# Optimization experiments

Measured on AMD Instinct MI355X. Metric: run time of the kernel, lower is better.

The kernel has to match this reference:

```python
import jax, jax.numpy as jnp
import numpy as np

# Ground-plane grid from proj_2DTo2D: W = 640/4 = 160, H = 480/4 = 120
GP_H, GP_W = 120, 160
PATCH_NUM = 1


def setup_inputs() -> dict:
    key = jax.random.key(0)
    k1, k2, k3 = jax.random.split(key, 3)
    nR, fh, fw, fdim = 4, 90, 160, 512  # 4 camera views, quarter-res feature maps
    nV = GP_H * GP_W  # 19200 ground-plane points per view
    inputs = jax.random.normal(k1, (nR, fh, fw, fdim), dtype=jnp.float32)
    # Projected image-plane coordinates (stand-in for calibration-based World2Image)
    im_x = jax.random.uniform(k2, (nR, nV), dtype=jnp.float32) * (fw - 1)
    im_y = jax.random.uniform(k3, (nR, nV), dtype=jnp.float32) * (fh - 1)
    return {"inputs": inputs, "im_x": im_x, "im_y": im_y}


def reference(inputs, im_x, im_y):
    # inputs: [nR, fh, fw, fdim]; im_x/im_y: [nR, nV] float pixel coords
    nR, fh, fw, fdim = inputs.shape
    im_x = jnp.clip(im_x, 0.0, fw - 1)
    im_y = jnp.clip(im_y, 0.0, fh - 1)
    x0 = jnp.floor(im_x).astype(jnp.int32)
    x1 = jnp.clip(x0 + 1, 0, fw - 1)
    y0 = jnp.floor(im_y).astype(jnp.int32)
    y1 = jnp.clip(y0 + 1, 0, fh - 1)
    x0f, x1f = x0.astype(im_x.dtype), x1.astype(im_x.dtype)
    y0f, y1f = y0.astype(im_y.dtype), y1.astype(im_y.dtype)

    b = jnp.arange(nR)[:, None]  # [nR, 1] batch index per grid point
    Ia = inputs[b, y0, x0]  # [nR, nV, fdim]
    Ib = inputs[b, y1, x0]
    Ic = inputs[b, y0, x1]
    Id = inputs[b, y1, x1]

    wa = ((x1f - im_x) * (y1f - im_y))[..., None]
    wb = ((x1f - im_x) * (im_y - y0f))[..., None]
    wc = ((im_x - x0f) * (y1f - im_y))[..., None]
    wd = ((im_x - x0f) * (im_y - y0f))[..., None]

    Ibilin = wa * Ia + wb * Ib + wc * Ic + wd * Id  # [nR, nV, fdim]
    return Ibilin.reshape(nR // PATCH_NUM, PATCH_NUM, GP_H, GP_W, fdim)
```

## Files before the change

kernel.cpp:

```cpp
#include <hip/hip_runtime.h>


typedef float f32x4 __attribute__((ext_vector_type(4)));

#define GLOBAL_AS __attribute__((address_space(1)))
#define LDS_AS    __attribute__((address_space(3)))

constexpr int NR   = 4;
constexpr int FH   = 90;
constexpr int FW   = 160;
constexpr int FDIM = 512;
constexpr int NV   = 120 * 160;
constexpr int NPTS = NR * NV;
constexpr int C4   = FDIM / 4;

constexpr int BY   = 2;
constexpr int BX   = 5;
constexpr int NGY  = FH / BY;
constexpr int NGX  = FW / BX;
constexpr int NBINS = NR * NGY * NGX;
constexpr int SY   = BY + 1;
constexpr int SX   = BX + 1;
constexpr int SCELLS = SY * SX;
constexpr int LDSX4 = SCELLS * C4;

constexpr int CAP   = 32;
constexpr int OVCAP = 4096;
constexpr int TPB   = 512;

__global__ void k_scatter(const float* __restrict__ imx, const float* __restrict__ imy,
                          int* __restrict__ binCnt, int* __restrict__ ovCnt,
                          int* __restrict__ perm, float2* __restrict__ sXY,
                          int* __restrict__ ovList) {
    int pt = blockIdx.x * blockDim.x + threadIdx.x;
    if (pt >= NPTS) return;
    int r = pt / NV;
    float x = fminf(fmaxf(imx[pt], 0.0f), (float)(FW - 1));
    float y = fminf(fmaxf(imy[pt], 0.0f), (float)(FH - 1));
    int b = (r * NGY + (int)floorf(y) / BY) * NGX + (int)floorf(x) / BX;
    int slot = atomicAdd(&binCnt[b], 1);
    if (slot < CAP) {
        int idx = b * CAP + slot;
        perm[idx] = pt;
        sXY[idx] = make_float2(x, y);
    } else {
        int o = atomicAdd(ovCnt, 1);
        if (o < OVCAP) ovList[o] = pt;
    }
}

__device__ __forceinline__ f32x4 lerp4(f32x4 A, f32x4 B, f32x4 C, f32x4 D,
                                       float wa, float wb, float wc, float wd) {
    return wa * A + wb * B + wc * C + wd * D;
}

__device__ __forceinline__ void weights_and_cells(float x, float y,
                                                  int& x0, int& x1, int& y0, int& y1,
                                                  float& wa, float& wb, float& wc, float& wd) {
    float x0f = floorf(x), y0f = floorf(y);
    x0 = (int)x0f; y0 = (int)y0f;
    x1 = min(x0 + 1, FW - 1);
    y1 = min(y0 + 1, FH - 1);
    float wx1 = (float)x1 - x;
    float wx0 = x - x0f;
    float wy1 = (float)y1 - y;
    float wy0 = y - y0f;
    wa = wx1 * wy1; wb = wx1 * wy0; wc = wx0 * wy1; wd = wx0 * wy0;
}

__global__ __launch_bounds__(TPB) void st_bins(
    const float* __restrict__ inp,
    const int* __restrict__ binCnt,
    const int* __restrict__ ovCnt,
    const int* __restrict__ perm,
    const float2* __restrict__ sXY,
    const int* __restrict__ ovList,
    const float* __restrict__ imx,
    const float* __restrict__ imy,
    float* __restrict__ out)
{
    __shared__ f32x4  lds[LDSX4];
    __shared__ int    pmS[CAP];
    __shared__ float2 xyS[CAP];

    int p = blockIdx.x;
    int b = (p & 7) * (NBINS >> 3) + (p >> 3);

    int r   = b / (NGY * NGX);
    int by0 = (b / NGX % NGY) * BY;
    int bx0 = (b % NGX) * BX;
    int tid = threadIdx.x;

    const f32x4* in4 = (const f32x4*)inp;
    int cnt  = min(binCnt[b], CAP);
    int base = b * CAP;

    #pragma unroll
    for (int i = 0; i < 5; ++i) {
        int idx = tid + i * TPB;
        if (idx < LDSX4) {
            int cell = idx >> 7;
            int c4   = idx & (C4 - 1);
            int ry   = cell / SX;
            int rx   = cell - ry * SX;
            int gy   = min(by0 + ry, FH - 1);
            int gx   = min(bx0 + rx, FW - 1);
            __builtin_amdgcn_global_load_lds(
                (const GLOBAL_AS void*)(in4 + (size_t)((r * FH + gy) * FW + gx) * C4 + c4),
                (LDS_AS void*)&lds[idx], 16, 0, 0);
        }
    }
    if (tid < cnt) {
        pmS[tid] = perm[base + tid];
        xyS[tid] = sXY[base + tid];
    }
    __syncthreads();

    int g  = tid >> 7;
    int c4 = tid & (C4 - 1);
    f32x4* out4 = (f32x4*)out;

    int i = g;
    for (; i + 4 < cnt; i += 8) {
        int    ptA = pmS[i];
        float2 cA  = xyS[i];
        int    ptB = pmS[i + 4];
        float2 cB  = xyS[i + 4];

        int x0A, x1A, y0A, y1A, x0B, x1B, y0B, y1B;
        float waA, wbA, wcA, wdA, waB, wbB, wcB, wdB;
        weights_and_cells(cA.x, cA.y, x0A, x1A, y0A, y1A, waA, wbA, wcA, wdA);
        weights_and_cells(cB.x, cB.y, x0B, x1B, y0B, y1B, waB, wbB, wcB, wdB);

        f32x4 Aa = lds[(((y0A - by0) * SX + (x0A - bx0)) << 7) + c4];
        f32x4 Ab = lds[(((y1A - by0) * SX + (x0A - bx0)) << 7) + c4];
        f32x4 Ac = lds[(((y0A - by0) * SX + (x1A - bx0)) << 7) + c4];
        f32x4 Ad = lds[(((y1A - by0) * SX + (x1A - bx0)) << 7) + c4];
        f32x4 Ba = lds[(((y0B - by0) * SX + (x0B - bx0)) << 7) + c4];
        f32x4 Bb = lds[(((y1B - by0) * SX + (x0B - bx0)) << 7) + c4];
        f32x4 Bc = lds[(((y0B - by0) * SX + (x1B - bx0)) << 7) + c4];
        f32x4 Bd = lds[(((y1B - by0) * SX + (x1B - bx0)) << 7) + c4];

        __builtin_nontemporal_store(lerp4(Aa, Ab, Ac, Ad, waA, wbA, wcA, wdA),
                                    out4 + (size_t)ptA * C4 + c4);
        __builtin_nontemporal_store(lerp4(Ba, Bb, Bc, Bd, waB, wbB, wcB, wdB),
                                    out4 + (size_t)ptB * C4 + c4);
    }
    if (i < cnt) {
        int    pt = pmS[i];
        float2 cc = xyS[i];
        int x0, x1, y0, y1; float wa, wb, wc, wd;
        weights_and_cells(cc.x, cc.y, x0, x1, y0, y1, wa, wb, wc, wd);
        f32x4 A = lds[(((y0 - by0) * SX + (x0 - bx0)) << 7) + c4];
        f32x4 B = lds[(((y1 - by0) * SX + (x0 - bx0)) << 7) + c4];
        f32x4 C = lds[(((y0 - by0) * SX + (x1 - bx0)) << 7) + c4];
        f32x4 D = lds[(((y1 - by0) * SX + (x1 - bx0)) << 7) + c4];
        __builtin_nontemporal_store(lerp4(A, B, C, D, wa, wb, wc, wd),
                                    out4 + (size_t)pt * C4 + c4);
    }

    int ov = min(*ovCnt, OVCAP);
    for (int j = b; j < ov; j += NBINS) {
        if (g != 0) continue;
        int pt = ovList[j];
        int rr = pt / NV;
        float x = fminf(fmaxf(imx[pt], 0.0f), (float)(FW - 1));
        float y = fminf(fmaxf(imy[pt], 0.0f), (float)(FH - 1));
        int x0, x1, y0, y1; float wa, wb, wc, wd;
        weights_and_cells(x, y, x0, x1, y0, y1, wa, wb, wc, wd);
        int rb = rr * FH;
        f32x4 A = in4[(size_t)((rb + y0) * FW + x0) * C4 + c4];
        f32x4 B = in4[(size_t)((rb + y1) * FW + x0) * C4 + c4];
        f32x4 C = in4[(size_t)((rb + y0) * FW + x1) * C4 + c4];
        f32x4 D = in4[(size_t)((rb + y1) * FW + x1) * C4 + c4];
        __builtin_nontemporal_store(lerp4(A, B, C, D, wa, wb, wc, wd),
                                    out4 + (size_t)pt * C4 + c4);
    }
}

__global__ __launch_bounds__(256) void st_bilinear_direct(
    const float* __restrict__ inp,
    const float* __restrict__ imx,
    const float* __restrict__ imy,
    float* __restrict__ out)
{
    int gid = blockIdx.x * blockDim.x + threadIdx.x;
    int pt = gid >> 7;
    int c4 = gid & (C4 - 1);
    if (pt >= NPTS) return;
    int r = pt / NV;
    float x = fminf(fmaxf(imx[pt], 0.0f), (float)(FW - 1));
    float y = fminf(fmaxf(imy[pt], 0.0f), (float)(FH - 1));
    int x0, x1, y0, y1; float wa, wb, wc, wd;
    weights_and_cells(x, y, x0, x1, y0, y1, wa, wb, wc, wd);
    const f32x4* base = (const f32x4*)inp;
    int rb = r * FH;
    f32x4 a = base[(size_t)((rb + y0) * FW + x0) * C4 + c4];
    f32x4 b = base[(size_t)((rb + y1) * FW + x0) * C4 + c4];
    f32x4 c = base[(size_t)((rb + y0) * FW + x1) * C4 + c4];
    f32x4 d = base[(size_t)((rb + y1) * FW + x1) * C4 + c4];
    ((f32x4*)out)[(size_t)pt * C4 + c4] = lerp4(a, b, c, d, wa, wb, wc, wd);
}

extern "C" void kernel_launch(void* const* d_in, const int* in_sizes, int n_in,
                              void* d_out, int out_size, void* d_ws, size_t ws_size,
                              hipStream_t stream) {
    const float* inp = (const float*)d_in[0];
    const float* imx = (const float*)d_in[1];
    const float* imy = (const float*)d_in[2];
    float* out = (float*)d_out;

    size_t need = (size_t)(NBINS + 1 + NBINS * CAP + OVCAP) * sizeof(int)
                + (size_t)NBINS * CAP * sizeof(float2);

    if (ws_size < need) {
        int nblocks = (NPTS * C4) / 256;
        hipLaunchKernelGGL(st_bilinear_direct, dim3(nblocks), dim3(256), 0, stream,
                           inp, imx, imy, out);
        return;
    }

    int*    binCnt = (int*)d_ws;
    int*    ovCnt  = binCnt + NBINS;
    int*    perm   = ovCnt + 1;
    float2* sXY    = (float2*)(perm + (size_t)NBINS * CAP);
    int*    ovList = (int*)(sXY + (size_t)NBINS * CAP);

    hipMemsetAsync(binCnt, 0, (NBINS + 1) * sizeof(int), stream);
    hipLaunchKernelGGL(k_scatter, dim3((NPTS + 255) / 256), dim3(256), 0, stream,
                       imx, imy, binCnt, ovCnt, perm, sXY, ovList);
    hipLaunchKernelGGL(st_bins, dim3(NBINS), dim3(TPB), 0, stream,
                       inp, binCnt, ovCnt, perm, sXY, ovList, imx, imy, out);
}
```

Baseline: 58.60 us.

## Fuse memset, scatter and binned bilinear into one cooperative persistent kernel

```diff
diff --git a/kernel.cpp b/kernel.cpp
--- a/kernel.cpp
+++ b/kernel.cpp
@@ -1,5 +1,8 @@
 #include <hip/hip_runtime.h>
-
+#include <hip/hip_cooperative_groups.h>
+
+
+namespace cg = cooperative_groups;
 
 typedef float f32x4 __attribute__((ext_vector_type(4)));
 
@@ -19,6 +22,7 @@
 constexpr int NGY  = FH / BY;
 constexpr int NGX  = FW / BX;
 constexpr int NBINS = NR * NGY * NGX;
+constexpr int NBX  = NBINS / 8;
 constexpr int SY   = BY + 1;
 constexpr int SX   = BX + 1;
 constexpr int SCELLS = SY * SX;
@@ -27,6 +31,181 @@
 constexpr int CAP   = 32;
 constexpr int OVCAP = 4096;
 constexpr int TPB   = 512;
+
+__device__ __forceinline__ f32x4 lerp4(f32x4 A, f32x4 B, f32x4 C, f32x4 D,
+                                       float wa, float wb, float wc, float wd) {
+    return wa * A + wb * B + wc * C + wd * D;
+}
+
+__device__ __forceinline__ void weights_and_cells(float x, float y,
+                                                  int& x0, int& x1, int& y0, int& y1,
+                                                  float& wa, float& wb, float& wc, float& wd) {
+    float x0f = floorf(x), y0f = floorf(y);
+    x0 = (int)x0f; y0 = (int)y0f;
+    x1 = min(x0 + 1, FW - 1);
+    y1 = min(y0 + 1, FH - 1);
+    float wx1 = (float)x1 - x;
+    float wx0 = x - x0f;
+    float wy1 = (float)y1 - y;
+    float wy0 = y - y0f;
+    wa = wx1 * wy1; wb = wx1 * wy0; wc = wx0 * wy1; wd = wx0 * wy0;
+}
+
+__device__ __forceinline__ void stage_bin_dev(const f32x4* __restrict__ in4,
+                                              f32x4* ldsbuf, int b, int tid) {
+    int r   = b / (NGY * NGX);
+    int by0 = (b / NGX % NGY) * BY;
+    int bx0 = (b % NGX) * BX;
+    #pragma unroll
+    for (int i = 0; i < 5; ++i) {
+        int idx = tid + i * TPB;
+        if (idx < LDSX4) {
+            int cell = idx >> 7;
+            int cc   = idx & (C4 - 1);
+            int ry   = cell / SX;
+            int rx   = cell - ry * SX;
+            int gy   = min(by0 + ry, FH - 1);
+            int gx   = min(bx0 + rx, FW - 1);
+            __builtin_amdgcn_global_load_lds(
+                (const GLOBAL_AS void*)(in4 + (size_t)((r * FH + gy) * FW + gx) * C4 + cc),
+                (LDS_AS void*)&ldsbuf[idx], 16, 0, 0);
+        }
+    }
+}
+
+__global__ __launch_bounds__(TPB) void st_fused(
+    const float* __restrict__ inp,
+    const float* __restrict__ imx,
+    const float* __restrict__ imy,
+    int* __restrict__ binCnt,
+    int* __restrict__ ovCnt,
+    int* __restrict__ perm,
+    float2* __restrict__ sXY,
+    int* __restrict__ ovList,
+    float* __restrict__ out)
+{
+    __shared__ f32x4  lds[LDSX4];
+    __shared__ int    pmS[CAP];
+    __shared__ float2 xyS[CAP];
+
+    cg::grid_group grid = cg::this_grid();
+    int nblk = gridDim.x;
+    int nthreads = nblk * TPB;
+    int bid = blockIdx.x;
+    int tid = threadIdx.x;
+    int gt  = bid * TPB + tid;
+
+    const f32x4* in4 = (const f32x4*)inp;
+
+    int xcd = bid & 7;
+    int s   = bid >> 3;
+    int bpx = nblk >> 3;
+    int s0  = (s * NBX) / bpx;
+    int s1  = ((s + 1) * NBX) / bpx;
+
+    for (int i = gt; i < NBINS + 1; i += nthreads) binCnt[i] = 0;
+    __threadfence();
+    grid.sync();
+
+    stage_bin_dev(in4, lds, xcd * NBX + s0, tid);
+
+    for (int pt = gt; pt < NPTS; pt += nthreads) {
+        int r = pt / NV;
+        float x = fminf(fmaxf(imx[pt], 0.0f), (float)(FW - 1));
+        float y = fminf(fmaxf(imy[pt], 0.0f), (float)(FH - 1));
+        int b = (r * NGY + (int)floorf(y) / BY) * NGX + (int)floorf(x) / BX;
+        int slot = atomicAdd(&binCnt[b], 1);
+        if (slot < CAP) {
+            int idx = b * CAP + slot;
+            perm[idx] = pt;
+            sXY[idx] = make_float2(x, y);
+        } else {
+            int o = atomicAdd(ovCnt, 1);
+            if (o < OVCAP) ovList[o] = pt;
+        }
+    }
+    __threadfence();
+    grid.sync();
+
+    f32x4* out4 = (f32x4*)out;
+    int g  = tid >> 7;
+    int c4 = tid & (C4 - 1);
+
+    for (int k = s0; k < s1; ++k) {
+        int b = xcd * NBX + k;
+        if (k > s0)
+            stage_bin_dev(in4, lds, b, tid);
+
+        int by0 = (b / NGX % NGY) * BY;
+        int bx0 = (b % NGX) * BX;
+        int cnt  = min(binCnt[b], CAP);
+        int base = b * CAP;
+        if (tid < cnt) {
+            pmS[tid] = perm[base + tid];
+            xyS[tid] = sXY[base + tid];
+        }
+        __syncthreads();
+
+        int i = g;
+        for (; i + 4 < cnt; i += 8) {
+            int    ptA = pmS[i];
+            float2 cA  = xyS[i];
+            int    ptB = pmS[i + 4];
+            float2 cB  = xyS[i + 4];
+
+            int x0A, x1A, y0A, y1A, x0B, x1B, y0B, y1B;
+            float waA, wbA, wcA, wdA, waB, wbB, wcB, wdB;
+            weights_and_cells(cA.x, cA.y, x0A, x1A, y0A, y1A, waA, wbA, wcA, wdA);
+            weights_and_cells(cB.x, cB.y, x0B, x1B, y0B, y1B, waB, wbB, wcB, wdB);
+
+            f32x4 Aa = lds[(((y0A - by0) * SX + (x0A - bx0)) << 7) + c4];
+            f32x4 Ab = lds[(((y1A - by0) * SX + (x0A - bx0)) << 7) + c4];
+            f32x4 Ac = lds[(((y0A - by0) * SX + (x1A - bx0)) << 7) + c4];
+            f32x4 Ad = lds[(((y1A - by0) * SX + (x1A - bx0)) << 7) + c4];
+            f32x4 Ba = lds[(((y0B - by0) * SX + (x0B - bx0)) << 7) + c4];
+            f32x4 Bb = lds[(((y1B - by0) * SX + (x0B - bx0)) << 7) + c4];
+            f32x4 Bc = lds[(((y0B - by0) * SX + (x1B - bx0)) << 7) + c4];
+            f32x4 Bd = lds[(((y1B - by0) * SX + (x1B - bx0)) << 7) + c4];
+
+            __builtin_nontemporal_store(lerp4(Aa, Ab, Ac, Ad, waA, wbA, wcA, wdA),
+                                        out4 + (size_t)ptA * C4 + c4);
+            __builtin_nontemporal_store(lerp4(Ba, Bb, Bc, Bd, waB, wbB, wcB, wdB),
+                                        out4 + (size_t)ptB * C4 + c4);
+        }
+        if (i < cnt) {
+            int    pt = pmS[i];
+            float2 cc = xyS[i];
+            int x0, x1, y0, y1; float wa, wb, wc, wd;
+            weights_and_cells(cc.x, cc.y, x0, x1, y0, y1, wa, wb, wc, wd);
+            f32x4 A = lds[(((y0 - by0) * SX + (x0 - bx0)) << 7) + c4];
+            f32x4 B = lds[(((y1 - by0) * SX + (x0 - bx0)) << 7) + c4];
+            f32x4 C = lds[(((y0 - by0) * SX + (x1 - bx0)) << 7) + c4];
+            f32x4 D = lds[(((y1 - by0) * SX + (x1 - bx0)) << 7) + c4];
+            __builtin_nontemporal_store(lerp4(A, B, C, D, wa, wb, wc, wd),
+                                        out4 + (size_t)pt * C4 + c4);
+        }
+        __syncthreads();
+    }
+
+    int ov = min(*ovCnt, OVCAP);
+    for (int j = bid; j < ov; j += nblk) {
+        if (g != 0) continue;
+        int pt = ovList[j];
+        int rr = pt / NV;
+        float x = fminf(fmaxf(imx[pt], 0.0f), (float)(FW - 1));
+        float y = fminf(fmaxf(imy[pt], 0.0f), (float)(FH - 1));
+        int x0, x1, y0, y1; float wa, wb, wc, wd;
+        weights_and_cells(x, y, x0, x1, y0, y1, wa, wb, wc, wd);
+        int rb = rr * FH;
+        f32x4 A = in4[(size_t)((rb + y0) * FW + x0) * C4 + c4];
+        f32x4 B = in4[(size_t)((rb + y1) * FW + x0) * C4 + c4];
+        f32x4 C = in4[(size_t)((rb + y0) * FW + x1) * C4 + c4];
+        f32x4 D = in4[(size_t)((rb + y1) * FW + x1) * C4 + c4];
+        __builtin_nontemporal_store(lerp4(A, B, C, D, wa, wb, wc, wd),
+                                    out4 + (size_t)pt * C4 + c4);
+    }
+}
+
 
 __global__ void k_scatter(const float* __restrict__ imx, const float* __restrict__ imy,
                           int* __restrict__ binCnt, int* __restrict__ ovCnt,
@@ -49,25 +228,6 @@
     }
 }
 
-__device__ __forceinline__ f32x4 lerp4(f32x4 A, f32x4 B, f32x4 C, f32x4 D,
-                                       float wa, float wb, float wc, float wd) {
-    return wa * A + wb * B + wc * C + wd * D;
-}
-
-__device__ __forceinline__ void weights_and_cells(float x, float y,
-                                                  int& x0, int& x1, int& y0, int& y1,
-                                                  float& wa, float& wb, float& wc, float& wd) {
-    float x0f = floorf(x), y0f = floorf(y);
-    x0 = (int)x0f; y0 = (int)y0f;
-    x1 = min(x0 + 1, FW - 1);
-    y1 = min(y0 + 1, FH - 1);
-    float wx1 = (float)x1 - x;
-    float wx0 = x - x0f;
-    float wy1 = (float)y1 - y;
-    float wy0 = y - y0f;
-    wa = wx1 * wy1; wb = wx1 * wy0; wc = wx0 * wy1; wd = wx0 * wy0;
-}
-
 __global__ __launch_bounds__(TPB) void st_bins(
     const float* __restrict__ inp,
     const int* __restrict__ binCnt,
@@ -86,7 +246,6 @@
     int p = blockIdx.x;
     int b = (p & 7) * (NBINS >> 3) + (p >> 3);
 
-    int r   = b / (NGY * NGX);
     int by0 = (b / NGX % NGY) * BY;
     int bx0 = (b % NGX) * BX;
     int tid = threadIdx.x;
@@ -95,21 +254,7 @@
     int cnt  = min(binCnt[b], CAP);
     int base = b * CAP;
 
-    #pragma unroll
-    for (int i = 0; i < 5; ++i) {
-        int idx = tid + i * TPB;
-        if (idx < LDSX4) {
-            int cell = idx >> 7;
-            int c4   = idx & (C4 - 1);
-            int ry   = cell / SX;
-            int rx   = cell - ry * SX;
-            int gy   = min(by0 + ry, FH - 1);
-            int gx   = min(bx0 + rx, FW - 1);
-            __builtin_amdgcn_global_load_lds(
-                (const GLOBAL_AS void*)(in4 + (size_t)((r * FH + gy) * FW + gx) * C4 + c4),
-                (LDS_AS void*)&lds[idx], 16, 0, 0);
-        }
-    }
+    stage_bin_dev(in4, lds, b, tid);
     if (tid < cnt) {
         pmS[tid] = perm[base + tid];
         xyS[tid] = sXY[base + tid];
@@ -210,8 +355,8 @@
     const float* imy = (const float*)d_in[2];
     float* out = (float*)d_out;
 
-    size_t need = (size_t)(NBINS + 1 + NBINS * CAP + OVCAP) * sizeof(int)
-                + (size_t)NBINS * CAP * sizeof(float2);
+    size_t need = (size_t)NBINS * CAP * sizeof(float2)
+                + (size_t)(NBINS * CAP + NBINS + 1 + OVCAP) * sizeof(int);
 
     if (ws_size < need) {
         int nblocks = (NPTS * C4) / 256;
@@ -220,13 +365,33 @@
         return;
     }
 
-    int*    binCnt = (int*)d_ws;
+    float2* sXY    = (float2*)d_ws;
+    int*    perm   = (int*)(sXY + (size_t)NBINS * CAP);
+    int*    binCnt = perm + (size_t)NBINS * CAP;
     int*    ovCnt  = binCnt + NBINS;
-    int*    perm   = ovCnt + 1;
-    float2* sXY    = (float2*)(perm + (size_t)NBINS * CAP);
-    int*    ovList = (int*)(sXY + (size_t)NBINS * CAP);
-
-    hipMemsetAsync(binCnt, 0, (NBINS + 1) * sizeof(int), stream);
+    int*    ovList = ovCnt + 1;
+
+    int dev = 0, coop = 0, ncu = 0, bpc = 0;
+    (void)hipGetDevice(&dev);
+    (void)hipDeviceGetAttribute(&coop, hipDeviceAttributeCooperativeLaunch, dev);
+    (void)hipDeviceGetAttribute(&ncu, hipDeviceAttributeMultiprocessorCount, dev);
+    hipError_t oe = hipOccupancyMaxActiveBlocksPerMultiprocessor(
+        &bpc, (const void*)st_fused, TPB, 0);
+
+    if (coop && oe == hipSuccess && ncu > 0 && bpc > 0) {
+        int nblk = (ncu * bpc) & ~7;
+        if (nblk > 1024) nblk = 1024;
+        if (nblk >= 8) {
+            void* args[] = { (void*)&inp, (void*)&imx, (void*)&imy,
+                             (void*)&binCnt, (void*)&ovCnt, (void*)&perm,
+                             (void*)&sXY, (void*)&ovList, (void*)&out };
+            hipError_t le = hipLaunchCooperativeKernel(
+                (const void*)st_fused, dim3(nblk), dim3(TPB), args, 0, stream);
+            if (le == hipSuccess) return;
+        }
+    }
+
+    (void)hipMemsetAsync(binCnt, 0, (NBINS + 1) * sizeof(int), stream);
     hipLaunchKernelGGL(k_scatter, dim3((NPTS + 255) / 256), dim3(256), 0, stream,
                        imx, imy, binCnt, ovCnt, perm, sXY, ovList);
     hipLaunchKernelGGL(st_bins, dim3(NBINS), dim3(TPB), 0, stream,
```

Result: slower. 214.9 us (+266.7%).

## Split each bin across two half-channel blocks and move overflow to separate kernel

Applied to the files above, without the earlier changes.

```diff
diff --git a/kernel.cpp b/kernel.cpp
--- a/kernel.cpp
+++ b/kernel.cpp
@@ -13,20 +13,22 @@
 constexpr int NV   = 120 * 160;
 constexpr int NPTS = NR * NV;
 constexpr int C4   = FDIM / 4;
+constexpr int H4   = C4 / 2;
 
 constexpr int BY   = 2;
 constexpr int BX   = 5;
 constexpr int NGY  = FH / BY;
 constexpr int NGX  = FW / BX;
 constexpr int NBINS = NR * NGY * NGX;
+constexpr int NB2  = NBINS * 2;
 constexpr int SY   = BY + 1;
 constexpr int SX   = BX + 1;
 constexpr int SCELLS = SY * SX;
-constexpr int LDSX4 = SCELLS * C4;
+constexpr int LDSH = SCELLS * H4;
 
 constexpr int CAP   = 32;
 constexpr int OVCAP = 4096;
-constexpr int TPB   = 512;
+constexpr int TPB   = 256;
 
 __global__ void k_scatter(const float* __restrict__ imx, const float* __restrict__ imy,
                           int* __restrict__ binCnt, int* __restrict__ ovCnt,
@@ -68,23 +70,23 @@
     wa = wx1 * wy1; wb = wx1 * wy0; wc = wx0 * wy1; wd = wx0 * wy0;
 }
 
-__global__ __launch_bounds__(TPB) void st_bins(
+__global__ __launch_bounds__(TPB) void st_bins_half(
     const float* __restrict__ inp,
     const int* __restrict__ binCnt,
     const int* __restrict__ ovCnt,
     const int* __restrict__ perm,
     const float2* __restrict__ sXY,
     const int* __restrict__ ovList,
-    const float* __restrict__ imx,
-    const float* __restrict__ imy,
     float* __restrict__ out)
 {
-    __shared__ f32x4  lds[LDSX4];
+    __shared__ f32x4  lds[LDSH];
     __shared__ int    pmS[CAP];
     __shared__ float2 xyS[CAP];
 
     int p = blockIdx.x;
-    int b = (p & 7) * (NBINS >> 3) + (p >> 3);
+    int l    = (p & 7) * (NB2 >> 3) + (p >> 3);
+    int b    = l >> 1;
+    int half = l & 1;
 
     int r   = b / (NGY * NGX);
     int by0 = (b / NGX % NGY) * BY;
@@ -94,19 +96,20 @@
     const f32x4* in4 = (const f32x4*)inp;
     int cnt  = min(binCnt[b], CAP);
     int base = b * CAP;
+    int hofs = half * H4;
 
     #pragma unroll
     for (int i = 0; i < 5; ++i) {
         int idx = tid + i * TPB;
-        if (idx < LDSX4) {
-            int cell = idx >> 7;
-            int c4   = idx & (C4 - 1);
+        if (idx < LDSH) {
+            int cell = idx >> 6;
+            int cc   = idx & (H4 - 1);
             int ry   = cell / SX;
             int rx   = cell - ry * SX;
             int gy   = min(by0 + ry, FH - 1);
             int gx   = min(bx0 + rx, FW - 1);
             __builtin_amdgcn_global_load_lds(
-                (const GLOBAL_AS void*)(in4 + (size_t)((r * FH + gy) * FW + gx) * C4 + c4),
+                (const GLOBAL_AS void*)(in4 + (size_t)((r * FH + gy) * FW + gx) * C4 + hofs + cc),
                 (LDS_AS void*)&lds[idx], 16, 0, 0);
         }
     }
@@ -116,8 +119,8 @@
     }
     __syncthreads();
 
-    int g  = tid >> 7;
-    int c4 = tid & (C4 - 1);
+    int g  = tid >> 6;
+    int cc = tid & (H4 - 1);
     f32x4* out4 = (f32x4*)out;
 
     int i = g;
@@ -132,50 +135,68 @@
         weights_and_cells(cA.x, cA.y, x0A, x1A, y0A, y1A, waA, wbA, wcA, wdA);
         weights_and_cells(cB.x, cB.y, x0B, x1B, y0B, y1B, waB, wbB, wcB, wdB);
 
-        f32x4 Aa = lds[(((y0A - by0) * SX + (x0A - bx0)) << 7) + c4];
-        f32x4 Ab = lds[(((y1A - by0) * SX + (x0A - bx0)) << 7) + c4];
-        f32x4 Ac = lds[(((y0A - by0) * SX + (x1A - bx0)) << 7) + c4];
-        f32x4 Ad = lds[(((y1A - by0) * SX + (x1A - bx0)) << 7) + c4];
-        f32x4 Ba = lds[(((y0B - by0) * SX + (x0B - bx0)) << 7) + c4];
-        f32x4 Bb = lds[(((y1B - by0) * SX + (x0B - bx0)) << 7) + c4];
-        f32x4 Bc = lds[(((y0B - by0) * SX + (x1B - bx0)) << 7) + c4];
-        f32x4 Bd = lds[(((y1B - by0) * SX + (x1B - bx0)) << 7) + c4];
+        f32x4 Aa = lds[(((y0A - by0) * SX + (x0A - bx0)) << 6) + cc];
+        f32x4 Ab = lds[(((y1A - by0) * SX + (x0A - bx0)) << 6) + cc];
+        f32x4 Ac = lds[(((y0A - by0) * SX + (x1A - bx0)) << 6) + cc];
+        f32x4 Ad = lds[(((y1A - by0) * SX + (x1A - bx0)) << 6) + cc];
+        f32x4 Ba = lds[(((y0B - by0) * SX + (x0B - bx0)) << 6) + cc];
+        f32x4 Bb = lds[(((y1B - by0) * SX + (x0B - bx0)) << 6) + cc];
+        f32x4 Bc = lds[(((y0B - by0) * SX + (x1B - bx0)) << 6) + cc];
+        f32x4 Bd = lds[(((y1B - by0) * SX + (x1B - bx0)) << 6) + cc];
 
         __builtin_nontemporal_store(lerp4(Aa, Ab, Ac, Ad, waA, wbA, wcA, wdA),
-                                    out4 + (size_t)ptA * C4 + c4);
+                                    out4 + (size_t)ptA * C4 + hofs + cc);
         __builtin_nontemporal_store(lerp4(Ba, Bb, Bc, Bd, waB, wbB, wcB, wdB),
-                                    out4 + (size_t)ptB * C4 + c4);
+                                    out4 + (size_t)ptB * C4 + hofs + cc);
     }
     if (i < cnt) {
         int    pt = pmS[i];
-        float2 cc = xyS[i];
+        float2 cx = xyS[i];
         int x0, x1, y0, y1; float wa, wb, wc, wd;
-        weights_and_cells(cc.x, cc.y, x0, x1, y0, y1, wa, wb, wc, wd);
-        f32x4 A = lds[(((y0 - by0) * SX + (x0 - bx0)) << 7) + c4];
-        f32x4 B = lds[(((y1 - by0) * SX + (x0 - bx0)) << 7) + c4];
-        f32x4 C = lds[(((y0 - by0) * SX + (x1 - bx0)) << 7) + c4];
-        f32x4 D = lds[(((y1 - by0) * SX + (x1 - bx0)) << 7) + c4];
+        weights_and_cells(cx.x, cx.y, x0, x1, y0, y1, wa, wb, wc, wd);
+        f32x4 A = lds[(((y0 - by0) * SX + (x0 - bx0)) << 6) + cc];
+        f32x4 B = lds[(((y1 - by0) * SX + (x0 - bx0)) << 6) + cc];
+        f32x4 C = lds[(((y0 - by0) * SX + (x1 - bx0)) << 6) + cc];
+        f32x4 D = lds[(((y1 - by0) * SX + (x1 - bx0)) << 6) + cc];
         __builtin_nontemporal_store(lerp4(A, B, C, D, wa, wb, wc, wd),
-                                    out4 + (size_t)pt * C4 + c4);
+                                    out4 + (size_t)pt * C4 + hofs + cc);
     }
 
     int ov = min(*ovCnt, OVCAP);
-    for (int j = b; j < ov; j += NBINS) {
-        if (g != 0) continue;
+    const f32x4* basep = in4;
+    for (int j = l >> 1; j < ov; j += NB2 >> 1) {
+        if (g != 0 || (l & 1) != half) continue;
         int pt = ovList[j];
         int rr = pt / NV;
-        float x = fminf(fmaxf(imx[pt], 0.0f), (float)(FW - 1));
-        float y = fminf(fmaxf(imy[pt], 0.0f), (float)(FH - 1));
-        int x0, x1, y0, y1; float wa, wb, wc, wd;
-        weights_and_cells(x, y, x0, x1, y0, y1, wa, wb, wc, wd);
-        int rb = rr * FH;
-        f32x4 A = in4[(size_t)((rb + y0) * FW + x0) * C4 + c4];
-        f32x4 B = in4[(size_t)((rb + y1) * FW + x0) * C4 + c4];
-        f32x4 C = in4[(size_t)((rb + y0) * FW + x1) * C4 + c4];
-        f32x4 D = in4[(size_t)((rb + y1) * FW + x1) * C4 + c4];
-        __builtin_nontemporal_store(lerp4(A, B, C, D, wa, wb, wc, wd),
-                                    out4 + (size_t)pt * C4 + c4);
-    }
+        (void)pt; (void)rr; (void)basep;
+    }
+}
+
+__global__ __launch_bounds__(TPB) void st_overflow(
+    const float* __restrict__ inp,
+    const float* __restrict__ imx,
+    const float* __restrict__ imy,
+    const int* __restrict__ ovCnt,
+    const int* __restrict__ ovList,
+    float* __restrict__ out)
+{
+    int ov = min(*ovCnt, OVCAP);
+    int slot = blockIdx.x * 2 + (threadIdx.x >> 7);
+    if (slot >= ov) return;
+    int c4 = threadIdx.x & (C4 - 1);
+    int pt = ovList[slot];
+    int r = pt / NV;
+    float x = fminf(fmaxf(imx[pt], 0.0f), (float)(FW - 1));
+    float y = fminf(fmaxf(imy[pt], 0.0f), (float)(FH - 1));
+    int x0, x1, y0, y1; float wa, wb, wc, wd;
+    weights_and_cells(x, y, x0, x1, y0, y1, wa, wb, wc, wd);
+    const f32x4* in4 = (const f32x4*)inp;
+    int rb = r * FH;
+    f32x4 A = in4[(size_t)((rb + y0) * FW + x0) * C4 + c4];
+    f32x4 B = in4[(size_t)((rb + y1) * FW + x0) * C4 + c4];
+    f32x4 C = in4[(size_t)((rb + y0) * FW + x1) * C4 + c4];
+    f32x4 D = in4[(size_t)((rb + y1) * FW + x1) * C4 + c4];
+    ((f32x4*)out)[(size_t)pt * C4 + c4] = lerp4(A, B, C, D, wa, wb, wc, wd);
 }
 
 __global__ __launch_bounds__(256) void st_bilinear_direct(
@@ -210,8 +231,8 @@
     const float* imy = (const float*)d_in[2];
     float* out = (float*)d_out;
 
-    size_t need = (size_t)(NBINS + 1 + NBINS * CAP + OVCAP) * sizeof(int)
-                + (size_t)NBINS * CAP * sizeof(float2);
+    size_t need = (size_t)NBINS * CAP * sizeof(float2)
+                + (size_t)(NBINS * CAP + NBINS + 1 + OVCAP) * sizeof(int);
 
     if (ws_size < need) {
         int nblocks = (NPTS * C4) / 256;
@@ -220,15 +241,17 @@
         return;
     }
 
-    int*    binCnt = (int*)d_ws;
+    float2* sXY    = (float2*)d_ws;
+    int*    perm   = (int*)(sXY + (size_t)NBINS * CAP);
+    int*    binCnt = perm + (size_t)NBINS * CAP;
     int*    ovCnt  = binCnt + NBINS;
-    int*    perm   = ovCnt + 1;
-    float2* sXY    = (float2*)(perm + (size_t)NBINS * CAP);
-    int*    ovList = (int*)(sXY + (size_t)NBINS * CAP);
-
-    hipMemsetAsync(binCnt, 0, (NBINS + 1) * sizeof(int), stream);
+    int*    ovList = ovCnt + 1;
+
+    (void)hipMemsetAsync(binCnt, 0, (NBINS + 1) * sizeof(int), stream);
     hipLaunchKernelGGL(k_scatter, dim3((NPTS + 255) / 256), dim3(256), 0, stream,
                        imx, imy, binCnt, ovCnt, perm, sXY, ovList);
-    hipLaunchKernelGGL(st_bins, dim3(NBINS), dim3(TPB), 0, stream,
-                       inp, binCnt, ovCnt, perm, sXY, ovList, imx, imy, out);
-}
+    hipLaunchKernelGGL(st_bins_half, dim3(NB2), dim3(TPB), 0, stream,
+                       inp, binCnt, ovCnt, perm, sXY, ovList, out);
+    hipLaunchKernelGGL(st_overflow, dim3(OVCAP / 2), dim3(TPB), 0, stream,
+                       inp, imx, imy, ovCnt, ovList, out);
+}
```

After: 60.50 us. +3.2%, slower.
